# Kernel tuning notes

Hardware: AMD Instinct MI355X
Metric: run time of the kernel (lower is better)

## Reference

```python
import jax, jax.numpy as jnp
import numpy as np

B, L, C, H = 8, 16384, 128, 4
EPS = 1e-5


def setup_inputs() -> dict:
    key = jax.random.key(0)
    k1, k2, k3, k4 = jax.random.split(key, 4)
    return {
        "x": jax.random.normal(k1, (B, L, C), dtype=jnp.float32),
        "W_qkv": jax.random.normal(k2, (3 * C, C), dtype=jnp.float32) * (C ** -0.5),
        "W_out": jax.random.normal(k3, (C, C), dtype=jnp.float32) * (C ** -0.5),
        "b_out": jax.random.normal(k4, (C,), dtype=jnp.float32) * 0.01,
        "gn_w": jnp.ones((C,), dtype=jnp.float32),
        "gn_b": jnp.zeros((C,), dtype=jnp.float32),
    }


def reference(x, W_qkv, W_out, b_out, gn_w, gn_b):
    b, l, c = x.shape
    h = H
    d = c // h                      # dim_head
    scale = d ** -0.5
    xc = jnp.swapaxes(x, 1, 2)      # [b, c, l]
    # 1x1 conv == channel matmul
    qkv = jnp.einsum('oc,bcl->bol', W_qkv, xc)     # [b, 3c, l]
    q, k, v = jnp.split(qkv, 3, axis=1)
    q = q.reshape(b, h, d, l)
    k = k.reshape(b, h, d, l)
    v = v.reshape(b, h, d, l)
    q = jax.nn.softmax(q, axis=2) * scale          # softmax over head-dim
    k = jax.nn.softmax(k, axis=3)                  # softmax over length
    context = jnp.einsum('bhcj,bhdj->bhcd', k, v)  # [b, h, d, d]
    out = jnp.einsum('bhcd,bhdi->bhci', context, q)  # [b, h, d, l]
    out = out.reshape(b, h * d, l)
    out = jnp.einsum('oc,bcl->bol', W_out, out) + b_out[None, :, None]
    # GroupNorm(1, c): normalize over (channel, length) per sample
    mean = jnp.mean(out, axis=(1, 2), keepdims=True)
    var = jnp.var(out, axis=(1, 2), keepdims=True)
    out = (out - mean) * jax.lax.rsqrt(var + EPS)
    out = out * gn_w[None, :, None] + gn_b[None, :, None]
    return jnp.swapaxes(out, 1, 2)                 # [b, l, c]
```

## Files before the change

kernel.cpp:

```cpp
#include <hip/hip_runtime.h>

#define BATCH 8
#define SEQL 16384
#define NCH 128
#define NH 4
#define HD 32
#define GEPS 1e-5f

typedef __bf16 bf16x8 __attribute__((ext_vector_type(8)));
typedef __bf16 bf16x4 __attribute__((ext_vector_type(4)));
typedef float f32x4 __attribute__((ext_vector_type(4)));

#define WKV_B   0
#define WQ_B    65536
#define WO_B    98304
#define CTXB_B  131072
#define CTXF_B  196608
#define ZF_B    327680
#define GNS_B   331776
#define GNF_B   331840
#define ZERO_BYTES (131072 + 4096 + 64 + 64)


__global__ void k_prep(const float* __restrict__ wqkv, const float* __restrict__ wout,
                       char* __restrict__ wsb) {
    int i = blockIdx.x * 256 + threadIdx.x;
    __bf16* wkvb = (__bf16*)(wsb + WKV_B);
    __bf16* wqb  = (__bf16*)(wsb + WQ_B);
    __bf16* wob  = (__bf16*)(wsb + WO_B);
    if (i < 384 * 128) {
        int o = i >> 7, c = i & 127;
        __bf16 v = (__bf16)wqkv[i];
        if (o < 128) wqb[o * 128 + c] = v;
        else         wkvb[(o - 128) * 128 + c] = v;
    }
    if (i < 128 * 128) wob[i] = (__bf16)wout[i];
}

__global__ __launch_bounds__(256, 2) void k_pass1(const float* __restrict__ x,
                                                  char* __restrict__ wsb) {
    __shared__ __attribute__((aligned(16))) __bf16 xb[8352];
    __shared__ __attribute__((aligned(16))) __bf16 ekv[16464];
    const int t = threadIdx.x;
    const int lane = t & 63, wave = t >> 6;
    const int n16 = lane & 15, q = lane >> 4;
    const int batch = blockIdx.x >> 6, sub = blockIdx.x & 63;
    const __bf16* __restrict__ wkvb = (const __bf16*)(wsb + WKV_B);

    bf16x8 aw[4][4];
#pragma unroll
    for (int mt = 0; mt < 4; mt++)
#pragma unroll
        for (int ks = 0; ks < 4; ks++)
            aw[mt][ks] = *(const bf16x8*)&wkvb[(wave * 64 + mt * 16 + n16) * 128 + ks * 32 + q * 8];

    f32x4 ctxacc[2][2];
#pragma unroll
    for (int i = 0; i < 2; i++)
#pragma unroll
        for (int j = 0; j < 2; j++) ctxacc[i][j] = (f32x4){0.f, 0.f, 0.f, 0.f};
    float zacc[4][4];
#pragma unroll
    for (int i = 0; i < 4; i++)
#pragma unroll
        for (int j = 0; j < 4; j++) zacc[i][j] = 0.f;

    for (int rep = 0; rep < 4; rep++) {
        const int chunk = sub + rep * 64;
        const float* xg = x + (size_t)(batch * SEQL + chunk * 64) * NCH;
#pragma unroll
        for (int r = 0; r < 8; r++) {
            int e = t + r * 256;
            int tok = e >> 5, c4 = (e & 31) * 4;
            float4 v = ((const float4*)xg)[e];
            bf16x4 h; h.x = (__bf16)v.x; h.y = (__bf16)v.y; h.z = (__bf16)v.z; h.w = (__bf16)v.w;
            *(bf16x4*)&xb[(c4 >> 5) * 2088 + ((c4 >> 3) & 3) * 520 + tok * 8 + (c4 & 7)] = h;
        }
        __syncthreads();
        f32x4 kvacc[4][4];
#pragma unroll
        for (int i = 0; i < 4; i++)
#pragma unroll
            for (int j = 0; j < 4; j++) kvacc[i][j] = (f32x4){0.f, 0.f, 0.f, 0.f};
#pragma unroll
        for (int ks = 0; ks < 4; ks++) {
            bf16x8 b[4];
#pragma unroll
            for (int nt = 0; nt < 4; nt++)
                b[nt] = *(const bf16x8*)&xb[ks * 2088 + q * 520 + (nt * 16 + n16) * 8];
#pragma unroll
            for (int mt = 0; mt < 4; mt++)
#pragma unroll
                for (int nt = 0; nt < 4; nt++)
                    kvacc[mt][nt] = __builtin_amdgcn_mfma_f32_16x16x32_bf16(
                        aw[mt][ks], b[nt], kvacc[mt][nt], 0, 0, 0);
        }
#pragma unroll
        for (int mt = 0; mt < 4; mt++)
#pragma unroll
            for (int nt = 0; nt < 4; nt++) {
                int tt = nt * 16 + n16;
                int base = (tt >> 5) * 8232 + ((tt >> 3) & 3) * 2056 + (tt & 7);
#pragma unroll
                for (int r = 0; r < 4; r++) {
                    float vv = kvacc[mt][nt][r];
                    if (wave < 2) { vv = __expf(vv); zacc[mt][r] += vv; }
                    int o = wave * 64 + mt * 16 + q * 4 + r;
                    ekv[base + o * 8] = (__bf16)vv;
                }
            }
        __syncthreads();
#pragma unroll
        for (int ks2 = 0; ks2 < 2; ks2++) {
            bf16x8 ea[2], vb[2];
#pragma unroll
            for (int ml = 0; ml < 2; ml++) {
                ea[ml] = *(const bf16x8*)&ekv[ks2 * 8232 + q * 2056 + (wave * 32 + ml * 16 + n16) * 8];
                vb[ml] = *(const bf16x8*)&ekv[ks2 * 8232 + q * 2056 + (128 + wave * 32 + ml * 16 + n16) * 8];
            }
#pragma unroll
            for (int ml = 0; ml < 2; ml++)
#pragma unroll
                for (int nl = 0; nl < 2; nl++)
                    ctxacc[ml][nl] = __builtin_amdgcn_mfma_f32_16x16x32_bf16(
                        ea[ml], vb[nl], ctxacc[ml][nl], 0, 0, 0);
        }
        __syncthreads();
    }
    float* ctxf = (float*)(wsb + CTXF_B) + ((size_t)(batch * 4 + wave) * 32) * 32;
#pragma unroll
    for (int ml = 0; ml < 2; ml++)
#pragma unroll
        for (int nl = 0; nl < 2; nl++)
#pragma unroll
            for (int r = 0; r < 4; r++)
                atomicAdd(&ctxf[(ml * 16 + q * 4 + r) * 32 + nl * 16 + n16], ctxacc[ml][nl][r]);
    if (wave < 2) {
        float* Zf = (float*)(wsb + ZF_B) + batch * 128;
#pragma unroll
        for (int mt = 0; mt < 4; mt++)
#pragma unroll
            for (int r = 0; r < 4; r++) {
                float z = zacc[mt][r];
                z += __shfl_xor(z, 1); z += __shfl_xor(z, 2);
                z += __shfl_xor(z, 4); z += __shfl_xor(z, 8);
                if (n16 == 0) atomicAdd(&Zf[wave * 64 + mt * 16 + q * 4 + r], z);
            }
    }
}

__global__ void k_ctxnorm(char* __restrict__ wsb) {
    int i = blockIdx.x * 256 + threadIdx.x;
    if (i < BATCH * NH * HD * HD) {
        const float* ctxf = (const float*)(wsb + CTXF_B);
        const float* Zf = (const float*)(wsb + ZF_B);
        __bf16* ctxb = (__bf16*)(wsb + CTXB_B);
        int c = (i >> 5) & 31, h = (i >> 10) & 3, b = i >> 12;
        ctxb[i] = (__bf16)(ctxf[i] / Zf[b * 128 + h * 32 + c]);
    }
}

__global__ __launch_bounds__(256, 2) void k_pass2(const float* __restrict__ x,
                                                  const float* __restrict__ bout,
                                                  char* __restrict__ wsb,
                                                  float* __restrict__ out) {
    __shared__ __attribute__((aligned(16))) __bf16 xb[8352];
    __shared__ __attribute__((aligned(16))) __bf16 pB[8352];
    __shared__ __attribute__((aligned(16))) __bf16 attB[8352];
    const int t = threadIdx.x;
    const int lane = t & 63, wave = t >> 6;
    const int n16 = lane & 15, q = lane >> 4;
    const int batch = blockIdx.x >> 6, sub = blockIdx.x & 63;
    const __bf16* __restrict__ wqb = (const __bf16*)(wsb + WQ_B);
    const __bf16* __restrict__ wob = (const __bf16*)(wsb + WO_B);
    const __bf16* __restrict__ ctxb = (const __bf16*)(wsb + CTXB_B);

    bf16x8 aq[2][4], ao[2][4];
#pragma unroll
    for (int ml = 0; ml < 2; ml++)
#pragma unroll
        for (int ks = 0; ks < 4; ks++) {
            aq[ml][ks] = *(const bf16x8*)&wqb[(wave * 32 + ml * 16 + n16) * 128 + ks * 32 + q * 8];
            ao[ml][ks] = *(const bf16x8*)&wob[(wave * 32 + ml * 16 + n16) * 128 + ks * 32 + q * 8];
        }
    bf16x8 actx[2];
#pragma unroll
    for (int ml = 0; ml < 2; ml++)
        actx[ml] = *(const bf16x8*)&ctxb[((size_t)(batch * 4 + wave) * 32 + ml * 16 + n16) * 32 + q * 8];
    float4 bias[2];
#pragma unroll
    for (int ml = 0; ml < 2; ml++)
        bias[ml] = *(const float4*)&bout[wave * 32 + ml * 16 + q * 4];

    float s1 = 0.f, s2 = 0.f;

    for (int rep = 0; rep < 4; rep++) {
        const int chunk = sub + rep * 64;
        const size_t tok0 = (size_t)batch * SEQL + chunk * 64;
        const float* xg = x + tok0 * NCH;
#pragma unroll
        for (int r = 0; r < 8; r++) {
            int e = t + r * 256;
            int tok = e >> 5, c4 = (e & 31) * 4;
            float4 v = ((const float4*)xg)[e];
            bf16x4 h; h.x = (__bf16)v.x; h.y = (__bf16)v.y; h.z = (__bf16)v.z; h.w = (__bf16)v.w;
            *(bf16x4*)&xb[(c4 >> 5) * 2088 + ((c4 >> 3) & 3) * 520 + tok * 8 + (c4 & 7)] = h;
        }
        __syncthreads();
        f32x4 qacc[2][4];
#pragma unroll
        for (int i = 0; i < 2; i++)
#pragma unroll
            for (int j = 0; j < 4; j++) qacc[i][j] = (f32x4){0.f, 0.f, 0.f, 0.f};
#pragma unroll
        for (int ks = 0; ks < 4; ks++) {
            bf16x8 b[4];
#pragma unroll
            for (int nt = 0; nt < 4; nt++)
                b[nt] = *(const bf16x8*)&xb[ks * 2088 + q * 520 + (nt * 16 + n16) * 8];
#pragma unroll
            for (int ml = 0; ml < 2; ml++)
#pragma unroll
                for (int nt = 0; nt < 4; nt++)
                    qacc[ml][nt] = __builtin_amdgcn_mfma_f32_16x16x32_bf16(
                        aq[ml][ks], b[nt], qacc[ml][nt], 0, 0, 0);
        }
#pragma unroll
        for (int nt = 0; nt < 4; nt++) {
            float ss = 0.f;
#pragma unroll
            for (int ml = 0; ml < 2; ml++)
#pragma unroll
                for (int r = 0; r < 4; r++) {
                    float e = __expf(qacc[ml][nt][r]);
                    qacc[ml][nt][r] = e;
                    ss += e;
                }
            ss += __shfl_xor(ss, 16);
            ss += __shfl_xor(ss, 32);
            float inv = 0.17677669529663687f / ss;
#pragma unroll
            for (int ml = 0; ml < 2; ml++)
#pragma unroll
                for (int r = 0; r < 4; r++) qacc[ml][nt][r] *= inv;
        }
#pragma unroll
        for (int ml = 0; ml < 2; ml++)
#pragma unroll
            for (int nt = 0; nt < 4; nt++) {
                bf16x4 h;
                h.x = (__bf16)qacc[ml][nt][0]; h.y = (__bf16)qacc[ml][nt][1];
                h.z = (__bf16)qacc[ml][nt][2]; h.w = (__bf16)qacc[ml][nt][3];
                *(bf16x4*)&pB[wave * 2088 + (ml * 2 + (q >> 1)) * 520 +
                              (nt * 16 + n16) * 8 + (q & 1) * 4] = h;
            }
        __syncthreads();
        f32x4 aacc[2][4];
#pragma unroll
        for (int ml = 0; ml < 2; ml++)
#pragma unroll
            for (int nt = 0; nt < 4; nt++) {
                bf16x8 pb = *(const bf16x8*)&pB[wave * 2088 + q * 520 + (nt * 16 + n16) * 8];
                aacc[ml][nt] = __builtin_amdgcn_mfma_f32_16x16x32_bf16(
                    actx[ml], pb, (f32x4){0.f, 0.f, 0.f, 0.f}, 0, 0, 0);
            }
#pragma unroll
        for (int ml = 0; ml < 2; ml++)
#pragma unroll
            for (int nt = 0; nt < 4; nt++) {
                bf16x4 h;
                h.x = (__bf16)aacc[ml][nt][0]; h.y = (__bf16)aacc[ml][nt][1];
                h.z = (__bf16)aacc[ml][nt][2]; h.w = (__bf16)aacc[ml][nt][3];
                *(bf16x4*)&attB[wave * 2088 + (ml * 2 + (q >> 1)) * 520 +
                                (nt * 16 + n16) * 8 + (q & 1) * 4] = h;
            }
        __syncthreads();
        f32x4 oacc[2][4];
#pragma unroll
        for (int i = 0; i < 2; i++)
#pragma unroll
            for (int j = 0; j < 4; j++) oacc[i][j] = (f32x4){0.f, 0.f, 0.f, 0.f};
#pragma unroll
        for (int ks = 0; ks < 4; ks++) {
            bf16x8 b[4];
#pragma unroll
            for (int nt = 0; nt < 4; nt++)
                b[nt] = *(const bf16x8*)&attB[ks * 2088 + q * 520 + (nt * 16 + n16) * 8];
#pragma unroll
            for (int ml = 0; ml < 2; ml++)
#pragma unroll
                for (int nt = 0; nt < 4; nt++)
                    oacc[ml][nt] = __builtin_amdgcn_mfma_f32_16x16x32_bf16(
                        ao[ml][ks], b[nt], oacc[ml][nt], 0, 0, 0);
        }
#pragma unroll
        for (int ml = 0; ml < 2; ml++)
#pragma unroll
            for (int nt = 0; nt < 4; nt++) {
                float4 vv;
                vv.x = oacc[ml][nt][0] + bias[ml].x;
                vv.y = oacc[ml][nt][1] + bias[ml].y;
                vv.z = oacc[ml][nt][2] + bias[ml].z;
                vv.w = oacc[ml][nt][3] + bias[ml].w;
                s1 += vv.x + vv.y + vv.z + vv.w;
                s2 += vv.x * vv.x + vv.y * vv.y + vv.z * vv.z + vv.w * vv.w;
                *(float4*)&out[(tok0 + nt * 16 + n16) * NCH + wave * 32 + ml * 16 + q * 4] = vv;
            }
        __syncthreads();
    }
#pragma unroll
    for (int off = 32; off > 0; off >>= 1) {
        s1 += __shfl_xor(s1, off);
        s2 += __shfl_xor(s2, off);
    }
    if (lane == 0) {
        float* gns = (float*)(wsb + GNS_B);
        atomicAdd(&gns[batch * 2 + 0], s1);
        atomicAdd(&gns[batch * 2 + 1], s2);
    }
}

__global__ void k_gnfinal(char* __restrict__ wsb) {
    int b = threadIdx.x;
    if (b < BATCH) {
        const float n = (float)NCH * (float)SEQL;
        const float* gns = (const float*)(wsb + GNS_B);
        float* gnf = (float*)(wsb + GNF_B);
        float mean = gns[b * 2] / n;
        float var = gns[b * 2 + 1] / n - mean * mean;
        gnf[b * 2] = mean;
        gnf[b * 2 + 1] = rsqrtf(var + GEPS);
    }
}

__global__ __launch_bounds__(256) void k_gnorm(float* __restrict__ out,
                                               const char* __restrict__ wsb,
                                               const float* __restrict__ gw,
                                               const float* __restrict__ gb) {
    size_t i4 = (size_t)blockIdx.x * 256 + threadIdx.x;
    int b = (int)(i4 >> 19);
    int c4 = (int)(i4 & 31);
    const float* gnf = (const float*)(wsb + GNF_B);
    float mean = gnf[b * 2], rstd = gnf[b * 2 + 1];
    float4 w = *(const float4*)&gw[c4 * 4];
    float4 bb = *(const float4*)&gb[c4 * 4];
    float4 v = ((float4*)out)[i4];
    v.x = (v.x - mean) * rstd * w.x + bb.x;
    v.y = (v.y - mean) * rstd * w.y + bb.y;
    v.z = (v.z - mean) * rstd * w.z + bb.z;
    v.w = (v.w - mean) * rstd * w.w + bb.w;
    ((float4*)out)[i4] = v;
}

extern "C" void kernel_launch(void* const* d_in, const int* in_sizes, int n_in,
                              void* d_out, int out_size, void* d_ws, size_t ws_size,
                              hipStream_t stream) {
    const float* x    = (const float*)d_in[0];
    const float* wqkv = (const float*)d_in[1];
    const float* wout = (const float*)d_in[2];
    const float* bout = (const float*)d_in[3];
    const float* gw   = (const float*)d_in[4];
    const float* gb   = (const float*)d_in[5];
    float* out = (float*)d_out;
    char* wsb  = (char*)d_ws;

    hipMemsetAsync(wsb + CTXF_B, 0, ZERO_BYTES, stream);
    k_prep<<<192, 256, 0, stream>>>(wqkv, wout, wsb);
    k_pass1<<<512, 256, 0, stream>>>(x, wsb);
    k_ctxnorm<<<128, 256, 0, stream>>>(wsb);
    k_pass2<<<512, 256, 0, stream>>>(x, bout, wsb, out);
    k_gnfinal<<<1, 64, 0, stream>>>(wsb);
    k_gnorm<<<16384, 256, 0, stream>>>(out, wsb, gw, gb);
}
```

Before: 230.3 us.

## Raise occupancy in both passes by splitting work into more, lighter blocks

Pass 1 now launches twice as many blocks with half the loop iterations. It loads the K/V weight fragments per k-step instead of holding all of them in registers, and it targets 3 blocks per CU. Pass 2 drops its loop and processes a single 64-token chunk per block, with 4x the blocks and two reused shared buffers instead of three. Block-level statistics are reduced through shared memory so each block issues one atomic pair. The goal is lower register and LDS pressure and better latency hiding, at the cost of more weight reloads from global/L2, more ctx atomics and less reuse of the weight registers per block.

```diff
diff --git a/kernel.cpp b/kernel.cpp
--- a/kernel.cpp
+++ b/kernel.cpp
@@ -20,7 +20,6 @@
 #define GNS_B   331776
 #define GNF_B   331840
 #define ZERO_BYTES (131072 + 4096 + 64 + 64)
-
 
 __global__ void k_prep(const float* __restrict__ wqkv, const float* __restrict__ wout,
                        char* __restrict__ wsb) {
@@ -37,22 +36,15 @@
     if (i < 128 * 128) wob[i] = (__bf16)wout[i];
 }
 
-__global__ __launch_bounds__(256, 2) void k_pass1(const float* __restrict__ x,
+__global__ __launch_bounds__(256, 3) void k_pass1(const float* __restrict__ x,
                                                   char* __restrict__ wsb) {
     __shared__ __attribute__((aligned(16))) __bf16 xb[8352];
     __shared__ __attribute__((aligned(16))) __bf16 ekv[16464];
     const int t = threadIdx.x;
     const int lane = t & 63, wave = t >> 6;
     const int n16 = lane & 15, q = lane >> 4;
-    const int batch = blockIdx.x >> 6, sub = blockIdx.x & 63;
+    const int batch = blockIdx.x >> 7, sub = blockIdx.x & 127;
     const __bf16* __restrict__ wkvb = (const __bf16*)(wsb + WKV_B);
-
-    bf16x8 aw[4][4];
-#pragma unroll
-    for (int mt = 0; mt < 4; mt++)
-#pragma unroll
-        for (int ks = 0; ks < 4; ks++)
-            aw[mt][ks] = *(const bf16x8*)&wkvb[(wave * 64 + mt * 16 + n16) * 128 + ks * 32 + q * 8];
 
     f32x4 ctxacc[2][2];
 #pragma unroll
@@ -65,9 +57,10 @@
 #pragma unroll
         for (int j = 0; j < 4; j++) zacc[i][j] = 0.f;
 
-    for (int rep = 0; rep < 4; rep++) {
-        const int chunk = sub + rep * 64;
+    for (int rep = 0; rep < 2; rep++) {
+        const int chunk = sub + rep * 128;
         const float* xg = x + (size_t)(batch * SEQL + chunk * 64) * NCH;
+        __syncthreads();
 #pragma unroll
         for (int r = 0; r < 8; r++) {
             int e = t + r * 256;
@@ -84,6 +77,10 @@
             for (int j = 0; j < 4; j++) kvacc[i][j] = (f32x4){0.f, 0.f, 0.f, 0.f};
 #pragma unroll
         for (int ks = 0; ks < 4; ks++) {
+            bf16x8 awk[4];
+#pragma unroll
+            for (int mt = 0; mt < 4; mt++)
+                awk[mt] = *(const bf16x8*)&wkvb[(wave * 64 + mt * 16 + n16) * 128 + ks * 32 + q * 8];
             bf16x8 b[4];
 #pragma unroll
             for (int nt = 0; nt < 4; nt++)
@@ -93,7 +90,7 @@
 #pragma unroll
                 for (int nt = 0; nt < 4; nt++)
                     kvacc[mt][nt] = __builtin_amdgcn_mfma_f32_16x16x32_bf16(
-                        aw[mt][ks], b[nt], kvacc[mt][nt], 0, 0, 0);
+                        awk[mt], b[nt], kvacc[mt][nt], 0, 0, 0);
         }
 #pragma unroll
         for (int mt = 0; mt < 4; mt++)
@@ -125,7 +122,6 @@
                     ctxacc[ml][nl] = __builtin_amdgcn_mfma_f32_16x16x32_bf16(
                         ea[ml], vb[nl], ctxacc[ml][nl], 0, 0, 0);
         }
-        __syncthreads();
     }
     float* ctxf = (float*)(wsb + CTXF_B) + ((size_t)(batch * 4 + wave) * 32) * 32;
 #pragma unroll
@@ -160,163 +156,154 @@
     }
 }
 
-__global__ __launch_bounds__(256, 2) void k_pass2(const float* __restrict__ x,
+__global__ __launch_bounds__(256, 4) void k_pass2(const float* __restrict__ x,
                                                   const float* __restrict__ bout,
                                                   char* __restrict__ wsb,
                                                   float* __restrict__ out) {
-    __shared__ __attribute__((aligned(16))) __bf16 xb[8352];
-    __shared__ __attribute__((aligned(16))) __bf16 pB[8352];
-    __shared__ __attribute__((aligned(16))) __bf16 attB[8352];
+    __shared__ __attribute__((aligned(16))) __bf16 bufA[8352];
+    __shared__ __attribute__((aligned(16))) __bf16 bufB[8352];
+    __shared__ float gred[8];
     const int t = threadIdx.x;
     const int lane = t & 63, wave = t >> 6;
     const int n16 = lane & 15, q = lane >> 4;
-    const int batch = blockIdx.x >> 6, sub = blockIdx.x & 63;
+    const int batch = blockIdx.x >> 8, chunk = blockIdx.x & 255;
     const __bf16* __restrict__ wqb = (const __bf16*)(wsb + WQ_B);
     const __bf16* __restrict__ wob = (const __bf16*)(wsb + WO_B);
     const __bf16* __restrict__ ctxb = (const __bf16*)(wsb + CTXB_B);
 
-    bf16x8 aq[2][4], ao[2][4];
-#pragma unroll
-    for (int ml = 0; ml < 2; ml++)
-#pragma unroll
-        for (int ks = 0; ks < 4; ks++) {
+    const size_t tok0 = (size_t)batch * SEQL + chunk * 64;
+    const float* xg = x + tok0 * NCH;
+#pragma unroll
+    for (int r = 0; r < 8; r++) {
+        int e = t + r * 256;
+        int tok = e >> 5, c4 = (e & 31) * 4;
+        float4 v = ((const float4*)xg)[e];
+        bf16x4 h; h.x = (__bf16)v.x; h.y = (__bf16)v.y; h.z = (__bf16)v.z; h.w = (__bf16)v.w;
+        *(bf16x4*)&bufA[(c4 >> 5) * 2088 + ((c4 >> 3) & 3) * 520 + tok * 8 + (c4 & 7)] = h;
+    }
+    bf16x8 aq[2][4];
+#pragma unroll
+    for (int ml = 0; ml < 2; ml++)
+#pragma unroll
+        for (int ks = 0; ks < 4; ks++)
             aq[ml][ks] = *(const bf16x8*)&wqb[(wave * 32 + ml * 16 + n16) * 128 + ks * 32 + q * 8];
-            ao[ml][ks] = *(const bf16x8*)&wob[(wave * 32 + ml * 16 + n16) * 128 + ks * 32 + q * 8];
-        }
     bf16x8 actx[2];
 #pragma unroll
     for (int ml = 0; ml < 2; ml++)
         actx[ml] = *(const bf16x8*)&ctxb[((size_t)(batch * 4 + wave) * 32 + ml * 16 + n16) * 32 + q * 8];
+    __syncthreads();
+
+    f32x4 qacc[2][4];
+#pragma unroll
+    for (int i = 0; i < 2; i++)
+#pragma unroll
+        for (int j = 0; j < 4; j++) qacc[i][j] = (f32x4){0.f, 0.f, 0.f, 0.f};
+#pragma unroll
+    for (int ks = 0; ks < 4; ks++) {
+        bf16x8 b[4];
+#pragma unroll
+        for (int nt = 0; nt < 4; nt++)
+            b[nt] = *(const bf16x8*)&bufA[ks * 2088 + q * 520 + (nt * 16 + n16) * 8];
+#pragma unroll
+        for (int ml = 0; ml < 2; ml++)
+#pragma unroll
+            for (int nt = 0; nt < 4; nt++)
+                qacc[ml][nt] = __builtin_amdgcn_mfma_f32_16x16x32_bf16(
+                    aq[ml][ks], b[nt], qacc[ml][nt], 0, 0, 0);
+    }
+#pragma unroll
+    for (int nt = 0; nt < 4; nt++) {
+        float ss = 0.f;
+#pragma unroll
+        for (int ml = 0; ml < 2; ml++)
+#pragma unroll
+            for (int r = 0; r < 4; r++) {
+                float e = __expf(qacc[ml][nt][r]);
+                qacc[ml][nt][r] = e;
+                ss += e;
+            }
+        ss += __shfl_xor(ss, 16);
+        ss += __shfl_xor(ss, 32);
+        float inv = 0.17677669529663687f / ss;
+#pragma unroll
+        for (int ml = 0; ml < 2; ml++)
+#pragma unroll
+            for (int r = 0; r < 4; r++) qacc[ml][nt][r] *= inv;
+    }
+    __syncthreads();
+#pragma unroll
+    for (int ml = 0; ml < 2; ml++)
+#pragma unroll
+        for (int nt = 0; nt < 4; nt++) {
+            bf16x4 h;
+            h.x = (__bf16)qacc[ml][nt][0]; h.y = (__bf16)qacc[ml][nt][1];
+            h.z = (__bf16)qacc[ml][nt][2]; h.w = (__bf16)qacc[ml][nt][3];
+            *(bf16x4*)&bufB[wave * 2088 + (ml * 2 + (q >> 1)) * 520 +
+                            (nt * 16 + n16) * 8 + (q & 1) * 4] = h;
+        }
+    __builtin_amdgcn_fence(__ATOMIC_ACQ_REL, "workgroup");
+#pragma unroll
+    for (int ml = 0; ml < 2; ml++)
+#pragma unroll
+        for (int nt = 0; nt < 4; nt++) {
+            bf16x8 pb = *(const bf16x8*)&bufB[wave * 2088 + q * 520 + (nt * 16 + n16) * 8];
+            f32x4 aacc = __builtin_amdgcn_mfma_f32_16x16x32_bf16(
+                actx[ml], pb, (f32x4){0.f, 0.f, 0.f, 0.f}, 0, 0, 0);
+            bf16x4 h;
+            h.x = (__bf16)aacc[0]; h.y = (__bf16)aacc[1];
+            h.z = (__bf16)aacc[2]; h.w = (__bf16)aacc[3];
+            *(bf16x4*)&bufA[wave * 2088 + (ml * 2 + (q >> 1)) * 520 +
+                            (nt * 16 + n16) * 8 + (q & 1) * 4] = h;
+        }
+    __syncthreads();
+    f32x4 oacc[2][4];
+#pragma unroll
+    for (int i = 0; i < 2; i++)
+#pragma unroll
+        for (int j = 0; j < 4; j++) oacc[i][j] = (f32x4){0.f, 0.f, 0.f, 0.f};
+#pragma unroll
+    for (int ks = 0; ks < 4; ks++) {
+        bf16x8 ao = *(const bf16x8*)&wob[(wave * 32 + 0 * 16 + n16) * 128 + ks * 32 + q * 8];
+        bf16x8 ao1 = *(const bf16x8*)&wob[(wave * 32 + 1 * 16 + n16) * 128 + ks * 32 + q * 8];
+        bf16x8 b[4];
+#pragma unroll
+        for (int nt = 0; nt < 4; nt++)
+            b[nt] = *(const bf16x8*)&bufA[ks * 2088 + q * 520 + (nt * 16 + n16) * 8];
+#pragma unroll
+        for (int nt = 0; nt < 4; nt++) {
+            oacc[0][nt] = __builtin_amdgcn_mfma_f32_16x16x32_bf16(ao, b[nt], oacc[0][nt], 0, 0, 0);
+            oacc[1][nt] = __builtin_amdgcn_mfma_f32_16x16x32_bf16(ao1, b[nt], oacc[1][nt], 0, 0, 0);
+        }
+    }
     float4 bias[2];
 #pragma unroll
     for (int ml = 0; ml < 2; ml++)
         bias[ml] = *(const float4*)&bout[wave * 32 + ml * 16 + q * 4];
-
     float s1 = 0.f, s2 = 0.f;
-
-    for (int rep = 0; rep < 4; rep++) {
-        const int chunk = sub + rep * 64;
-        const size_t tok0 = (size_t)batch * SEQL + chunk * 64;
-        const float* xg = x + tok0 * NCH;
-#pragma unroll
-        for (int r = 0; r < 8; r++) {
-            int e = t + r * 256;
-            int tok = e >> 5, c4 = (e & 31) * 4;
-            float4 v = ((const float4*)xg)[e];
-            bf16x4 h; h.x = (__bf16)v.x; h.y = (__bf16)v.y; h.z = (__bf16)v.z; h.w = (__bf16)v.w;
-            *(bf16x4*)&xb[(c4 >> 5) * 2088 + ((c4 >> 3) & 3) * 520 + tok * 8 + (c4 & 7)] = h;
-        }
-        __syncthreads();
-        f32x4 qacc[2][4];
-#pragma unroll
-        for (int i = 0; i < 2; i++)
-#pragma unroll
-            for (int j = 0; j < 4; j++) qacc[i][j] = (f32x4){0.f, 0.f, 0.f, 0.f};
-#pragma unroll
-        for (int ks = 0; ks < 4; ks++) {
-            bf16x8 b[4];
-#pragma unroll
-            for (int nt = 0; nt < 4; nt++)
-                b[nt] = *(const bf16x8*)&xb[ks * 2088 + q * 520 + (nt * 16 + n16) * 8];
-#pragma unroll
-            for (int ml = 0; ml < 2; ml++)
-#pragma unroll
-                for (int nt = 0; nt < 4; nt++)
-                    qacc[ml][nt] = __builtin_amdgcn_mfma_f32_16x16x32_bf16(
-                        aq[ml][ks], b[nt], qacc[ml][nt], 0, 0, 0);
-        }
+#pragma unroll
+    for (int ml = 0; ml < 2; ml++)
 #pragma unroll
         for (int nt = 0; nt < 4; nt++) {
-            float ss = 0.f;
-#pragma unroll
-            for (int ml = 0; ml < 2; ml++)
-#pragma unroll
-                for (int r = 0; r < 4; r++) {
-                    float e = __expf(qacc[ml][nt][r]);
-                    qacc[ml][nt][r] = e;
-                    ss += e;
-                }
-            ss += __shfl_xor(ss, 16);
-            ss += __shfl_xor(ss, 32);
-            float inv = 0.17677669529663687f / ss;
-#pragma unroll
-            for (int ml = 0; ml < 2; ml++)
-#pragma unroll
-                for (int r = 0; r < 4; r++) qacc[ml][nt][r] *= inv;
-        }
-#pragma unroll
-        for (int ml = 0; ml < 2; ml++)
-#pragma unroll
-            for (int nt = 0; nt < 4; nt++) {
-                bf16x4 h;
-                h.x = (__bf16)qacc[ml][nt][0]; h.y = (__bf16)qacc[ml][nt][1];
-                h.z = (__bf16)qacc[ml][nt][2]; h.w = (__bf16)qacc[ml][nt][3];
-                *(bf16x4*)&pB[wave * 2088 + (ml * 2 + (q >> 1)) * 520 +
-                              (nt * 16 + n16) * 8 + (q & 1) * 4] = h;
-            }
-        __syncthreads();
-        f32x4 aacc[2][4];
-#pragma unroll
-        for (int ml = 0; ml < 2; ml++)
-#pragma unroll
-            for (int nt = 0; nt < 4; nt++) {
-                bf16x8 pb = *(const bf16x8*)&pB[wave * 2088 + q * 520 + (nt * 16 + n16) * 8];
-                aacc[ml][nt] = __builtin_amdgcn_mfma_f32_16x16x32_bf16(
-                    actx[ml], pb, (f32x4){0.f, 0.f, 0.f, 0.f}, 0, 0, 0);
-            }
-#pragma unroll
-        for (int ml = 0; ml < 2; ml++)
-#pragma unroll
-            for (int nt = 0; nt < 4; nt++) {
-                bf16x4 h;
-                h.x = (__bf16)aacc[ml][nt][0]; h.y = (__bf16)aacc[ml][nt][1];
-                h.z = (__bf16)aacc[ml][nt][2]; h.w = (__bf16)aacc[ml][nt][3];
-                *(bf16x4*)&attB[wave * 2088 + (ml * 2 + (q >> 1)) * 520 +
-                                (nt * 16 + n16) * 8 + (q & 1) * 4] = h;
-            }
-        __syncthreads();
-        f32x4 oacc[2][4];
-#pragma unroll
-        for (int i = 0; i < 2; i++)
-#pragma unroll
-            for (int j = 0; j < 4; j++) oacc[i][j] = (f32x4){0.f, 0.f, 0.f, 0.f};
-#pragma unroll
-        for (int ks = 0; ks < 4; ks++) {
-            bf16x8 b[4];
-#pragma unroll
-            for (int nt = 0; nt < 4; nt++)
-                b[nt] = *(const bf16x8*)&attB[ks * 2088 + q * 520 + (nt * 16 + n16) * 8];
-#pragma unroll
-            for (int ml = 0; ml < 2; ml++)
-#pragma unroll
-                for (int nt = 0; nt < 4; nt++)
-                    oacc[ml][nt] = __builtin_amdgcn_mfma_f32_16x16x32_bf16(
-                        ao[ml][ks], b[nt], oacc[ml][nt], 0, 0, 0);
-        }
-#pragma unroll
-        for (int ml = 0; ml < 2; ml++)
-#pragma unroll
-            for (int nt = 0; nt < 4; nt++) {
-                float4 vv;
-                vv.x = oacc[ml][nt][0] + bias[ml].x;
-                vv.y = oacc[ml][nt][1] + bias[ml].y;
-                vv.z = oacc[ml][nt][2] + bias[ml].z;
-                vv.w = oacc[ml][nt][3] + bias[ml].w;
-                s1 += vv.x + vv.y + vv.z + vv.w;
-                s2 += vv.x * vv.x + vv.y * vv.y + vv.z * vv.z + vv.w * vv.w;
-                *(float4*)&out[(tok0 + nt * 16 + n16) * NCH + wave * 32 + ml * 16 + q * 4] = vv;
-            }
-        __syncthreads();
-    }
+            float4 vv;
+            vv.x = oacc[ml][nt][0] + bias[ml].x;
+            vv.y = oacc[ml][nt][1] + bias[ml].y;
+            vv.z = oacc[ml][nt][2] + bias[ml].z;
+            vv.w = oacc[ml][nt][3] + bias[ml].w;
+            s1 += vv.x + vv.y + vv.z + vv.w;
+            s2 += vv.x * vv.x + vv.y * vv.y + vv.z * vv.z + vv.w * vv.w;
+            *(float4*)&out[(tok0 + nt * 16 + n16) * NCH + wave * 32 + ml * 16 + q * 4] = vv;
+        }
 #pragma unroll
     for (int off = 32; off > 0; off >>= 1) {
         s1 += __shfl_xor(s1, off);
         s2 += __shfl_xor(s2, off);
     }
-    if (lane == 0) {
+    if (lane == 0) { gred[wave] = s1; gred[4 + wave] = s2; }
+    __syncthreads();
+    if (t == 0) {
         float* gns = (float*)(wsb + GNS_B);
-        atomicAdd(&gns[batch * 2 + 0], s1);
-        atomicAdd(&gns[batch * 2 + 1], s2);
+        atomicAdd(&gns[batch * 2 + 0], gred[0] + gred[1] + gred[2] + gred[3]);
+        atomicAdd(&gns[batch * 2 + 1], gred[4] + gred[5] + gred[6] + gred[7]);
     }
 }
 
@@ -366,9 +353,9 @@
 
     hipMemsetAsync(wsb + CTXF_B, 0, ZERO_BYTES, stream);
     k_prep<<<192, 256, 0, stream>>>(wqkv, wout, wsb);
-    k_pass1<<<512, 256, 0, stream>>>(x, wsb);
+    k_pass1<<<1024, 256, 0, stream>>>(x, wsb);
     k_ctxnorm<<<128, 256, 0, stream>>>(wsb);
-    k_pass2<<<512, 256, 0, stream>>>(x, bout, wsb, out);
+    k_pass2<<<2048, 256, 0, stream>>>(x, bout, wsb, out);
     k_gnfinal<<<1, 64, 0, stream>>>(wsb);
     k_gnorm<<<16384, 256, 0, stream>>>(out, wsb, gw, gb);
 }
```

After: 282.3 us. +22.6%, slower.
